# Optimization experiments

Measured on AMD Instinct MI355X. Metric: run time of the kernel, lower is better.

## Reference

```python
import jax, jax.numpy as jnp
import numpy as np

B, S, H = 32, 2048, 1024


def setup_inputs() -> dict:
    key = jax.random.key(0)
    ks = jax.random.split(key, 8)
    scale = 1.0 / np.sqrt(H)
    return {
        "query": jax.random.normal(ks[0], (B, 1, H), dtype=jnp.float32),
        "keys": jax.random.normal(ks[1], (B, S, H), dtype=jnp.float32),
        "Wa_w": jax.random.uniform(ks[2], (H, H), jnp.float32, -scale, scale),
        "Wa_b": jax.random.uniform(ks[3], (H,), jnp.float32, -scale, scale),
        "Ua_w": jax.random.uniform(ks[4], (H, H), jnp.float32, -scale, scale),
        "Ua_b": jax.random.uniform(ks[5], (H,), jnp.float32, -scale, scale),
        "Va_w": jax.random.uniform(ks[6], (1, H), jnp.float32, -scale, scale),
        "Va_b": jax.random.uniform(ks[7], (1,), jnp.float32, -scale, scale),
        "idx": 0,
    }


def reference(query, keys, Wa_w, Wa_b, Ua_w, Ua_b, Va_w, Va_b, idx):
    # torch Linear: y = x @ W.T + b
    q_proj = jnp.einsum("bqh,oh->bqo", query, Wa_w) + Wa_b   # (B,1,H)
    k_proj = jnp.einsum("bsh,oh->bso", keys, Ua_w) + Ua_b    # (B,S,H)
    energy = jnp.tanh(q_proj + k_proj)                        # (B,S,H) broadcast over S
    scores = jnp.einsum("bsh,h->bs", energy, Va_w[0]) + Va_b[0]  # (B,S)
    weights = jax.nn.softmax(scores, axis=-1)[:, None, :]     # (B,1,S)
    context = jnp.einsum("bqs,bsh->bqh", weights, keys)       # (B,1,H)
    return (context, weights)
```

## Files before the change

kernel.cpp:

```cpp
#include <hip/hip_runtime.h>
#include <hip/hip_bf16.h>
#include <math.h>


#define B_ 32
#define S_ 2048
#define H_ 1024
#define M_ (B_ * S_)

#define QP_BLOCKS 512
#define UA_BLOCKS 32

typedef __bf16 bf16x8 __attribute__((ext_vector_type(8)));
typedef float floatx4 __attribute__((ext_vector_type(4)));

__device__ inline unsigned bf16_rne(float f) {
  unsigned u = __builtin_bit_cast(unsigned, f);
  return (u + 0x7fffu + ((u >> 16) & 1u)) >> 16;
}
__device__ inline unsigned pk2(float x, float y) {
  return bf16_rne(x) | (bf16_rne(y) << 16);
}
__device__ inline unsigned cvtpk(float x, float y) {
  unsigned r;
  asm("v_cvt_pk_bf16_f32 %0, %1, %2" : "=v"(r) : "v"(x), "v"(y));
  return r;
}

__device__ inline float fast_tanh(float x) {
  const float xc = fminf(fmaxf(x, -8.f), 8.f);
  const float e = __expf(2.f * xc);
  return (e - 1.f) * __builtin_amdgcn_rcpf(e + 1.f);
}

#define GLDS(g, l)                                                    \
  __builtin_amdgcn_global_load_lds(                                   \
      (const __attribute__((address_space(1))) void*)(g),             \
      (__attribute__((address_space(3))) void*)(l), 16, 0, 0)

__device__ inline uint4 conv8(const float4* s2) {
  const float4 a = s2[0], b = s2[1];
  uint4 o;
  o.x = pk2(a.x, a.y); o.y = pk2(a.z, a.w);
  o.z = pk2(b.x, b.y); o.w = pk2(b.z, b.w);
  return o;
}

__global__ __launch_bounds__(256) void prep_kernel(
    const float* __restrict__ Ua_w, const float* __restrict__ query,
    const float* __restrict__ Wa_w, const float* __restrict__ Wa_b,
    const float* __restrict__ Ua_b, unsigned short* __restrict__ ubf,
    float* __restrict__ qp, int do_ua) {
  const int blk = blockIdx.x;
  const int tid = threadIdx.x;
  if (blk < QP_BLOCKS) {
    const int b = blk >> 4;
    const int os = (blk & 15) * 64;
    const int lane = tid & 63;
    const int w = tid >> 6;
    __shared__ float qsh[H_];
    *(float4*)&qsh[tid * 4] = *(const float4*)(query + (size_t)b * H_ + tid * 4);
    __syncthreads();
    for (int t = 0; t < 16; ++t) {
      const int o = os + w * 16 + t;
      const float* wr = Wa_w + (size_t)o * H_;
      float p = 0.f;
#pragma unroll
      for (int j = 0; j < 16; ++j) p += wr[lane + 64 * j] * qsh[lane + 64 * j];
#pragma unroll
      for (int m = 32; m; m >>= 1) p += __shfl_xor(p, m);
      if (lane == 0) qp[b * H_ + o] = p + Wa_b[o] + Ua_b[o];
    }
  } else {
    if (!do_ua) return;
    const int tg = (blk - QP_BLOCKS) * 256 + tid;
#pragma unroll
    for (int c = 0; c < 16; ++c) {
      const size_t idx = (size_t)c * 8192 + tg;
      ((uint4*)ubf)[idx] = conv8((const float4*)Ua_w + idx * 2);
    }
  }
}

__device__ inline void swizzle_rc(int idx, int& rb, int& cb) {
  cb = (idx >> 3) & 7;
  rb = (idx & 7) | ((idx >> 6) << 3);
}
__device__ inline int chunk_f(int r) { return (r & 3) ^ ((r >> 2) & 3); }

__global__ __launch_bounds__(256) void scores_af32_kernel(
    const float* __restrict__ keys, const unsigned short* __restrict__ ubf,
    const float* __restrict__ qp, const float* __restrict__ Va_w,
    float* __restrict__ sp) {
  const int tid = threadIdx.x;
  int rb, cb;
  swizzle_rc(blockIdx.x, rb, cb);
  const int row0 = rb * 128, c0 = cb * 128;
  const int bq = row0 >> 11;
  const int lane = tid & 63;
  const int w = tid >> 6;
  const int wm = w >> 1, wn = w & 1;
  const int q4 = lane >> 4, n16 = lane & 15;

  __shared__ __align__(16) float Asmf[128][32];
  __shared__ __align__(16) unsigned short Bsm[128][32];
  __shared__ float red[2][128];

  floatx4 acc[4][4];
#pragma unroll
  for (int i = 0; i < 4; ++i)
#pragma unroll
    for (int j = 0; j < 4; ++j) acc[i][j] = {0.f, 0.f, 0.f, 0.f};

  const int r0a = w * 32;

  const int lr = lane >> 2;
  const int lc = ((lane & 3) ^ chunk_f(lr)) * 8;
  const unsigned short* gB0 = ubf + (size_t)(c0 + r0a + lr) * H_ + lc;
  const unsigned short* gB1 = ubf + (size_t)(c0 + r0a + 16 + lr) * H_ + lc;
  unsigned short* lB0 = &Bsm[r0a][0];
  unsigned short* lB1 = &Bsm[r0a + 16][0];

  const int arow = lane >> 3;
  const int achk = ((lane & 7) ^ arow) * 4;
  const float* gA0 = keys + (size_t)(row0 + r0a + 0 + arow) * H_ + achk;
  const float* gA1 = keys + (size_t)(row0 + r0a + 8 + arow) * H_ + achk;
  const float* gA2 = keys + (size_t)(row0 + r0a + 16 + arow) * H_ + achk;
  const float* gA3 = keys + (size_t)(row0 + r0a + 24 + arow) * H_ + achk;
  float* lA0 = &Asmf[r0a + 0][0];
  float* lA1 = &Asmf[r0a + 8][0];
  float* lA2 = &Asmf[r0a + 16][0];
  float* lA3 = &Asmf[r0a + 24][0];

  const int fn = chunk_f(n16);
  const int fa = n16 & 7;
  const int ac0f = (((q4 << 1) ^ fa)) << 2;
  const int ac1f = (((q4 << 1) | 1) ^ fa) << 2;

  for (int kt = 0; kt < 32; ++kt) {
    const int k0 = kt * 32;
    __syncthreads();
    GLDS(gA0 + k0, lA0);
    GLDS(gA1 + k0, lA1);
    GLDS(gA2 + k0, lA2);
    GLDS(gA3 + k0, lA3);
    GLDS(gB0 + k0, lB0);
    GLDS(gB1 + k0, lB1);
    __syncthreads();
    bf16x8 af[4], bfr[4];
#pragma unroll
    for (int i = 0; i < 4; ++i) {
      const float* ar = &Asmf[wm * 64 + i * 16 + n16][0];
      const float4 x0 = *(const float4*)(ar + ac0f);
      const float4 x1 = *(const float4*)(ar + ac1f);
      uint4 u;
      u.x = cvtpk(x0.x, x0.y); u.y = cvtpk(x0.z, x0.w);
      u.z = cvtpk(x1.x, x1.y); u.w = cvtpk(x1.z, x1.w);
      af[i] = __builtin_bit_cast(bf16x8, u);
    }
#pragma unroll
    for (int j = 0; j < 4; ++j)
      bfr[j] = *(const bf16x8*)&Bsm[wn * 64 + j * 16 + n16][(q4 ^ fn) * 8];
#pragma unroll
    for (int i = 0; i < 4; ++i)
#pragma unroll
      for (int j = 0; j < 4; ++j)
        acc[i][j] = __builtin_amdgcn_mfma_f32_16x16x32_bf16(af[i], bfr[j], acc[i][j], 0, 0, 0);
  }

  float rsum[4][4];
#pragma unroll
  for (int i = 0; i < 4; ++i)
#pragma unroll
    for (int r = 0; r < 4; ++r) rsum[i][r] = 0.f;
#pragma unroll
  for (int j = 0; j < 4; ++j) {
    const int col = c0 + wn * 64 + j * 16 + n16;
    const float qv = qp[bq * H_ + col];
    const float vv = Va_w[col];
#pragma unroll
    for (int i = 0; i < 4; ++i)
#pragma unroll
      for (int r = 0; r < 4; ++r)
        rsum[i][r] += fast_tanh(acc[i][j][r] + qv) * vv;
  }
#pragma unroll
  for (int i = 0; i < 4; ++i)
#pragma unroll
    for (int r = 0; r < 4; ++r) {
      float v = rsum[i][r];
      v += __shfl_xor(v, 1);
      v += __shfl_xor(v, 2);
      v += __shfl_xor(v, 4);
      v += __shfl_xor(v, 8);
      rsum[i][r] = v;
    }
  if (n16 == 0) {
#pragma unroll
    for (int i = 0; i < 4; ++i)
#pragma unroll
      for (int r = 0; r < 4; ++r)
        red[wn][wm * 64 + i * 16 + q4 * 4 + r] = rsum[i][r];
  }
  __syncthreads();
  if (tid < 128) sp[(size_t)cb * M_ + row0 + tid] = red[0][tid] + red[1][tid];
}

__global__ __launch_bounds__(256) void scores_f32_kernel(
    const float* __restrict__ keys, const float* __restrict__ Ua_w,
    const float* __restrict__ qp, const float* __restrict__ Va_w,
    float* __restrict__ sp) {
  const int tid = threadIdx.x;
  int rb, cb;
  swizzle_rc(blockIdx.x, rb, cb);
  const int row0 = rb * 128, c0 = cb * 128;
  const int bq = row0 >> 11;
  const int lane = tid & 63;
  const int w = tid >> 6;
  const int wm = w >> 1, wn = w & 1;
  const int q4 = lane >> 4, n16 = lane & 15;

  __shared__ __align__(16) unsigned short Asm[128][40];
  __shared__ __align__(16) unsigned short Bsm[128][40];
  __shared__ float red[2][128];

  floatx4 acc[4][4];
#pragma unroll
  for (int i = 0; i < 4; ++i)
#pragma unroll
    for (int j = 0; j < 4; ++j) acc[i][j] = {0.f, 0.f, 0.f, 0.f};

  for (int kt = 0; kt < 32; ++kt) {
    const int k0 = kt * 32;
    __syncthreads();
#pragma unroll
    for (int rep = 0; rep < 4; ++rep) {
      const int idx4 = rep * 256 + tid;
      const int r = idx4 >> 3;
      const int c4 = (idx4 & 7) << 2;
      const float4 va = *(const float4*)(keys + (size_t)(row0 + r) * H_ + k0 + c4);
      *(uint2*)&Asm[r][c4] = make_uint2(pk2(va.x, va.y), pk2(va.z, va.w));
      const float4 vb = *(const float4*)(Ua_w + (size_t)(c0 + r) * H_ + k0 + c4);
      *(uint2*)&Bsm[r][c4] = make_uint2(pk2(vb.x, vb.y), pk2(vb.z, vb.w));
    }
    __syncthreads();
    bf16x8 af[4], bfr[4];
#pragma unroll
    for (int i = 0; i < 4; ++i)
      af[i] = *(const bf16x8*)&Asm[wm * 64 + i * 16 + n16][q4 * 8];
#pragma unroll
    for (int j = 0; j < 4; ++j)
      bfr[j] = *(const bf16x8*)&Bsm[wn * 64 + j * 16 + n16][q4 * 8];
#pragma unroll
    for (int i = 0; i < 4; ++i)
#pragma unroll
      for (int j = 0; j < 4; ++j)
        acc[i][j] = __builtin_amdgcn_mfma_f32_16x16x32_bf16(af[i], bfr[j], acc[i][j], 0, 0, 0);
  }

  float rsum[4][4];
#pragma unroll
  for (int i = 0; i < 4; ++i)
#pragma unroll
    for (int r = 0; r < 4; ++r) rsum[i][r] = 0.f;
#pragma unroll
  for (int j = 0; j < 4; ++j) {
    const int col = c0 + wn * 64 + j * 16 + n16;
    const float qv = qp[bq * H_ + col];
    const float vv = Va_w[col];
#pragma unroll
    for (int i = 0; i < 4; ++i)
#pragma unroll
      for (int r = 0; r < 4; ++r)
        rsum[i][r] += fast_tanh(acc[i][j][r] + qv) * vv;
  }
#pragma unroll
  for (int i = 0; i < 4; ++i)
#pragma unroll
    for (int r = 0; r < 4; ++r) {
      float v = rsum[i][r];
      v += __shfl_xor(v, 1);
      v += __shfl_xor(v, 2);
      v += __shfl_xor(v, 4);
      v += __shfl_xor(v, 8);
      rsum[i][r] = v;
    }
  if (n16 == 0) {
#pragma unroll
    for (int i = 0; i < 4; ++i)
#pragma unroll
      for (int r = 0; r < 4; ++r)
        red[wn][wm * 64 + i * 16 + q4 * 4 + r] = rsum[i][r];
  }
  __syncthreads();
  if (tid < 128) sp[(size_t)cb * M_ + row0 + tid] = red[0][tid] + red[1][tid];
}

__global__ __launch_bounds__(256) void softmax_kernel(
    const float* __restrict__ sp, float* __restrict__ sw) {
  const int b = blockIdx.x, tid = threadIdx.x;
  float v[8];
#pragma unroll
  for (int k = 0; k < 8; ++k) {
    const size_t base = (size_t)b * S_ + tid + 256 * k;
    float s = 0.f;
#pragma unroll
    for (int j = 0; j < 8; ++j) s += sp[(size_t)j * M_ + base];
    v[k] = s;
  }
  float mx = v[0];
#pragma unroll
  for (int k = 1; k < 8; ++k) mx = fmaxf(mx, v[k]);
#pragma unroll
  for (int m = 32; m; m >>= 1) mx = fmaxf(mx, __shfl_xor(mx, m));
  __shared__ float sred[4], ssum[4];
  if ((tid & 63) == 0) sred[tid >> 6] = mx;
  __syncthreads();
  mx = fmaxf(fmaxf(sred[0], sred[1]), fmaxf(sred[2], sred[3]));
  float e[8], s = 0.f;
#pragma unroll
  for (int k = 0; k < 8; ++k) { e[k] = __expf(v[k] - mx); s += e[k]; }
#pragma unroll
  for (int m = 32; m; m >>= 1) s += __shfl_xor(s, m);
  if ((tid & 63) == 0) ssum[tid >> 6] = s;
  __syncthreads();
  s = ssum[0] + ssum[1] + ssum[2] + ssum[3];
  const float inv = 1.0f / s;
#pragma unroll
  for (int k = 0; k < 8; ++k) sw[b * S_ + tid + 256 * k] = e[k] * inv;
}

__global__ __launch_bounds__(256) void context1_kernel(
    const float* __restrict__ keys, const float* __restrict__ weights,
    float* __restrict__ pctx) {
  const int b = blockIdx.x >> 6;
  const int ch = blockIdx.x & 63;
  const int s0 = ch * 32;
  const int h4 = threadIdx.x;
  const float4* kp4 = (const float4*)(keys + (size_t)(b * S_ + s0) * H_) + h4;
  const float4* wp4 = (const float4*)(weights + b * S_ + s0);
  float4 acc = {0.f, 0.f, 0.f, 0.f};
#pragma unroll
  for (int sq = 0; sq < 8; ++sq) {
    const float4 wv = wp4[sq];
    const float4 k0 = kp4[(sq * 4 + 0) * 256];
    const float4 k1 = kp4[(sq * 4 + 1) * 256];
    const float4 k2 = kp4[(sq * 4 + 2) * 256];
    const float4 k3 = kp4[(sq * 4 + 3) * 256];
    acc.x += wv.x * k0.x + wv.y * k1.x + wv.z * k2.x + wv.w * k3.x;
    acc.y += wv.x * k0.y + wv.y * k1.y + wv.z * k2.y + wv.w * k3.y;
    acc.z += wv.x * k0.z + wv.y * k1.z + wv.z * k2.z + wv.w * k3.z;
    acc.w += wv.x * k0.w + wv.y * k1.w + wv.z * k2.w + wv.w * k3.w;
  }
  *(float4*)(pctx + ((size_t)(b * 64 + ch)) * H_ + h4 * 4) = acc;
}

__global__ __launch_bounds__(256) void context2_kernel(
    const float* __restrict__ pctx, float* __restrict__ ctx) {
  const int b = blockIdx.x;
  const int h4 = threadIdx.x * 4;
  float4 acc = {0.f, 0.f, 0.f, 0.f};
#pragma unroll 8
  for (int c = 0; c < 64; ++c) {
    const float4 v = *(const float4*)(pctx + ((size_t)(b * 64 + c)) * H_ + h4);
    acc.x += v.x; acc.y += v.y; acc.z += v.z; acc.w += v.w;
  }
  *(float4*)(ctx + b * H_ + h4) = acc;
}

extern "C" void kernel_launch(void* const* d_in, const int* in_sizes, int n_in,
                              void* d_out, int out_size, void* d_ws, size_t ws_size,
                              hipStream_t stream) {
  const float* query = (const float*)d_in[0];
  const float* keys  = (const float*)d_in[1];
  const float* Wa_w  = (const float*)d_in[2];
  const float* Wa_b  = (const float*)d_in[3];
  const float* Ua_w  = (const float*)d_in[4];
  const float* Ua_b  = (const float*)d_in[5];
  const float* Va_w  = (const float*)d_in[6];

  float* out = (float*)d_out;
  float* ctx = out;
  float* sw  = out + B_ * H_;

  const size_t qpb = (size_t)B_ * H_ * 4;
  const size_t spb = (size_t)8 * M_ * 4;
  const size_t pcb = (size_t)B_ * 64 * H_ * 4;
  const size_t ub  = (size_t)H_ * H_ * 2;
  float* qp = (float*)d_ws;
  float* sp = (float*)((char*)d_ws + qpb);
  float* pctx = (float*)((char*)d_ws + qpb + spb);
  unsigned short* ubf = (unsigned short*)((char*)d_ws + qpb + spb + pcb);
  const bool fast = ws_size >= qpb + spb + pcb + ub;

  prep_kernel<<<QP_BLOCKS + UA_BLOCKS, 256, 0, stream>>>(
      Ua_w, query, Wa_w, Wa_b, Ua_b, ubf, qp, fast ? 1 : 0);
  if (fast) {
    scores_af32_kernel<<<4096, 256, 0, stream>>>(keys, ubf, qp, Va_w, sp);
  } else {
    scores_f32_kernel<<<4096, 256, 0, stream>>>(keys, Ua_w, qp, Va_w, sp);
  }
  softmax_kernel<<<B_, 256, 0, stream>>>(sp, sw);
  context1_kernel<<<2048, 256, 0, stream>>>(keys, sw, pctx);
  context2_kernel<<<B_, 256, 0, stream>>>(pctx, ctx);
}
```

Measured before the change: 640.0 us.

## Double-buffer LDS tiles in scores GEMM to overlap loads with MFMA

Splits the shared-memory A and B tiles into two buffers and issues the global-to-LDS loads for the next K tile before computing on the current one, with a single barrier per iteration. This is meant to hide global memory latency behind MFMA work, which the old load-sync-compute loop could not. It doubles LDS use per block, which may reduce occupancy, and adds a barrier before the reduction writes.

Result: slower. 704.2 us (+10.0%).

```diff
diff --git a/kernel.cpp b/kernel.cpp
--- a/kernel.cpp
+++ b/kernel.cpp
@@ -102,9 +102,11 @@
   const int wm = w >> 1, wn = w & 1;
   const int q4 = lane >> 4, n16 = lane & 15;
 
-  __shared__ __align__(16) float Asmf[128][32];
-  __shared__ __align__(16) unsigned short Bsm[128][32];
+  __shared__ __align__(16) float Asmf[2][128][32];
+  __shared__ __align__(16) unsigned short Bsm[2][128][32];
   __shared__ float red[2][128];
+  const int BUFA = 128 * 32;
+  const int BUFB = 128 * 32;
 
   floatx4 acc[4][4];
 #pragma unroll
@@ -118,8 +120,8 @@
   const int lc = ((lane & 3) ^ chunk_f(lr)) * 8;
   const unsigned short* gB0 = ubf + (size_t)(c0 + r0a + lr) * H_ + lc;
   const unsigned short* gB1 = ubf + (size_t)(c0 + r0a + 16 + lr) * H_ + lc;
-  unsigned short* lB0 = &Bsm[r0a][0];
-  unsigned short* lB1 = &Bsm[r0a + 16][0];
+  unsigned short* lB0 = &Bsm[0][r0a][0];
+  unsigned short* lB1 = &Bsm[0][r0a + 16][0];
 
   const int arow = lane >> 3;
   const int achk = ((lane & 7) ^ arow) * 4;
@@ -127,46 +129,62 @@
   const float* gA1 = keys + (size_t)(row0 + r0a + 8 + arow) * H_ + achk;
   const float* gA2 = keys + (size_t)(row0 + r0a + 16 + arow) * H_ + achk;
   const float* gA3 = keys + (size_t)(row0 + r0a + 24 + arow) * H_ + achk;
-  float* lA0 = &Asmf[r0a + 0][0];
-  float* lA1 = &Asmf[r0a + 8][0];
-  float* lA2 = &Asmf[r0a + 16][0];
-  float* lA3 = &Asmf[r0a + 24][0];
+  float* lA0 = &Asmf[0][r0a + 0][0];
+  float* lA1 = &Asmf[0][r0a + 8][0];
+  float* lA2 = &Asmf[0][r0a + 16][0];
+  float* lA3 = &Asmf[0][r0a + 24][0];
 
   const int fn = chunk_f(n16);
   const int fa = n16 & 7;
   const int ac0f = (((q4 << 1) ^ fa)) << 2;
   const int ac1f = (((q4 << 1) | 1) ^ fa) << 2;
 
-  for (int kt = 0; kt < 32; ++kt) {
-    const int k0 = kt * 32;
+#define STAGE(k0, ao, bo)                 \
+  do {                                    \
+    GLDS(gA0 + (k0), lA0 + (ao));         \
+    GLDS(gA1 + (k0), lA1 + (ao));         \
+    GLDS(gA2 + (k0), lA2 + (ao));         \
+    GLDS(gA3 + (k0), lA3 + (ao));         \
+    GLDS(gB0 + (k0), lB0 + (bo));         \
+    GLDS(gB1 + (k0), lB1 + (bo));         \
+  } while (0)
+
+#define COMPUTE(buf)                                                           \
+  do {                                                                         \
+    bf16x8 af[4], bfr[4];                                                      \
+    _Pragma("unroll") for (int i = 0; i < 4; ++i) {                            \
+      const float* ar = &Asmf[buf][wm * 64 + i * 16 + n16][0];                 \
+      const float4 x0 = *(const float4*)(ar + ac0f);                           \
+      const float4 x1 = *(const float4*)(ar + ac1f);                           \
+      uint4 u;                                                                 \
+      u.x = cvtpk(x0.x, x0.y); u.y = cvtpk(x0.z, x0.w);                        \
+      u.z = cvtpk(x1.x, x1.y); u.w = cvtpk(x1.z, x1.w);                        \
+      af[i] = __builtin_bit_cast(bf16x8, u);                                   \
+    }                                                                          \
+    _Pragma("unroll") for (int j = 0; j < 4; ++j)                              \
+      bfr[j] = *(const bf16x8*)&Bsm[buf][wn * 64 + j * 16 + n16][(q4 ^ fn) * 8]; \
+    _Pragma("unroll") for (int i = 0; i < 4; ++i)                              \
+      _Pragma("unroll") for (int j = 0; j < 4; ++j)                            \
+        acc[i][j] = __builtin_amdgcn_mfma_f32_16x16x32_bf16(af[i], bfr[j],     \
+                                                            acc[i][j], 0, 0, 0); \
+  } while (0)
+
+  STAGE(0, 0, 0);
+  __syncthreads();
+
+  int cur = 0;
+  for (int kt = 0; kt < 31; ++kt) {
+    const int nxt = cur ^ 1;
+    STAGE((kt + 1) * 32, nxt * BUFA, nxt * BUFB);
+    __builtin_amdgcn_sched_barrier(0);
+    COMPUTE(cur);
     __syncthreads();
-    GLDS(gA0 + k0, lA0);
-    GLDS(gA1 + k0, lA1);
-    GLDS(gA2 + k0, lA2);
-    GLDS(gA3 + k0, lA3);
-    GLDS(gB0 + k0, lB0);
-    GLDS(gB1 + k0, lB1);
-    __syncthreads();
-    bf16x8 af[4], bfr[4];
-#pragma unroll
-    for (int i = 0; i < 4; ++i) {
-      const float* ar = &Asmf[wm * 64 + i * 16 + n16][0];
-      const float4 x0 = *(const float4*)(ar + ac0f);
-      const float4 x1 = *(const float4*)(ar + ac1f);
-      uint4 u;
-      u.x = cvtpk(x0.x, x0.y); u.y = cvtpk(x0.z, x0.w);
-      u.z = cvtpk(x1.x, x1.y); u.w = cvtpk(x1.z, x1.w);
-      af[i] = __builtin_bit_cast(bf16x8, u);
-    }
-#pragma unroll
-    for (int j = 0; j < 4; ++j)
-      bfr[j] = *(const bf16x8*)&Bsm[wn * 64 + j * 16 + n16][(q4 ^ fn) * 8];
-#pragma unroll
-    for (int i = 0; i < 4; ++i)
-#pragma unroll
-      for (int j = 0; j < 4; ++j)
-        acc[i][j] = __builtin_amdgcn_mfma_f32_16x16x32_bf16(af[i], bfr[j], acc[i][j], 0, 0, 0);
-  }
+    cur = nxt;
+  }
+  COMPUTE(cur);
+
+#undef STAGE
+#undef COMPUTE
 
   float rsum[4][4];
 #pragma unroll
@@ -195,6 +213,7 @@
       v += __shfl_xor(v, 8);
       rsum[i][r] = v;
     }
+  __syncthreads();
   if (n16 == 0) {
 #pragma unroll
     for (int i = 0; i < 4; ++i)
```
